# Kernel optimization log

Hardware: AMD Instinct MI355X
Metric: run time of the kernel (lower is better)

The kernel has to match this reference:

```python
import jax, jax.numpy as jnp
from jax import lax
import numpy as np

B, HW, C = 32, 4096, 256
G = 32            # factor / groups
CG = C // G       # per-group channels = 8
EPS = 1e-5


def setup_inputs() -> dict:
    key = jax.random.key(0)
    ks = jax.random.split(key, 7)
    s = 1.0 / np.sqrt(CG)
    s3 = 1.0 / np.sqrt(CG * 9)
    return {
        "x": jax.random.normal(ks[0], (B, HW, C), dtype=jnp.float32),
        "w1": jax.random.uniform(ks[1], (CG, CG), jnp.float32, -s, s),        # conv1x1 weight (O,I)
        "b1": jax.random.uniform(ks[2], (CG,), jnp.float32, -s, s),
        "w3": jax.random.uniform(ks[3], (CG, CG, 3, 3), jnp.float32, -s3, s3),  # conv3x3 weight (O,I,kH,kW)
        "b3": jax.random.uniform(ks[4], (CG,), jnp.float32, -s3, s3),
        "gn_w": jnp.ones((CG,), jnp.float32),
        "gn_b": jnp.zeros((CG,), jnp.float32),
    }


def reference(x, w1, b1, w3, b3, gn_w, gn_b):
    b, hw, c = x.shape
    h = int(np.sqrt(hw)); w = h
    cg = c // G
    n = b * G
    # (b, hw, c) -> (b, c, h, w) -> (b*G, cg, h, w)
    gx = x.transpose(0, 2, 1).reshape(b, c, h, w).reshape(n, cg, h, w)

    # directional pooling
    x_h = gx.mean(axis=3, keepdims=True)                       # (n,cg,h,1)
    x_w = gx.mean(axis=2, keepdims=True).transpose(0, 1, 3, 2)  # (n,cg,w,1)
    cat = jnp.concatenate([x_h, x_w], axis=2)                  # (n,cg,h+w,1)
    # 1x1 conv == channel matmul
    hwm = jnp.einsum('oi,nipq->nopq', w1, cat) + b1[None, :, None, None]
    xh, xw = hwm[:, :, :h], hwm[:, :, h:]

    gated = gx * jax.nn.sigmoid(xh) * jax.nn.sigmoid(xw.transpose(0, 1, 3, 2))

    # GroupNorm(cg groups over cg channels) == per-channel norm over spatial dims
    mu = gated.mean(axis=(2, 3), keepdims=True)
    var = gated.var(axis=(2, 3), keepdims=True)
    x1 = (gated - mu) * lax.rsqrt(var + EPS) * gn_w[None, :, None, None] + gn_b[None, :, None, None]

    x2 = lax.conv_general_dilated(gx, w3, (1, 1), ((1, 1), (1, 1)),
                                  dimension_numbers=('NCHW', 'OIHW', 'NCHW')) + b3[None, :, None, None]

    x11 = jax.nn.softmax(x1.mean(axis=(2, 3)), axis=-1)[:, None, :]  # (n,1,cg)
    x21 = jax.nn.softmax(x2.mean(axis=(2, 3)), axis=-1)[:, None, :]  # (n,1,cg)
    x12 = x2.reshape(n, cg, h * w)
    x22 = x1.reshape(n, cg, h * w)

    weights = (x11 @ x12 + x21 @ x22).reshape(n, 1, h, w)
    out = (gx * jax.nn.sigmoid(weights)).reshape(b, c, h, w)
    return out.reshape(b, c, hw).transpose(0, 2, 1)
```

## Files before the change

### kernel.cpp

```cpp
#include <hip/hip_runtime.h>
#include <math.h>


#define NBLK 1024
#define NTHR 512
#define CSTR 2052

typedef unsigned int uint;

__device__ __forceinline__ uint pk2(float a, float b) {
    uint ua = __builtin_bit_cast(uint, a);
    uint ub = __builtin_bit_cast(uint, b);
    ua = (ua + 0x7FFFu + ((ua >> 16) & 1u)) >> 16;
    ub = (ub + 0x7FFFu + ((ub >> 16) & 1u)) >> 16;
    return ua | (ub << 16);
}
__device__ __forceinline__ float blo(uint u) { return __builtin_bit_cast(float, u << 16); }
__device__ __forceinline__ float bhi(uint u) { return __builtin_bit_cast(float, u & 0xFFFF0000u); }
__device__ __forceinline__ float sigm(float v) { return 1.0f / (1.0f + __expf(-v)); }

__global__ __launch_bounds__(512, 4) void fused_ema_kernel(
    const float* __restrict__ x,
    const float* __restrict__ w1,
    const float* __restrict__ b1,
    const float* __restrict__ w3,
    const float* __restrict__ b3,
    const float* __restrict__ gn_w,
    const float* __restrict__ gn_b,
    float* __restrict__ out)
{
    __shared__ __align__(16) uint  gxp[8 * CSTR];
    __shared__ __align__(16) float sg[8 * 128];
    __shared__ __align__(16) float uni[1024];
    __shared__ __align__(16) float t1s[512];
    __shared__ __align__(16) float weff[96];
    __shared__ float Ti[8], m2s[8], Ai[8], Ci[8], x11s[8], x21s[8];
    __shared__ float wconst_s;

    const int t = threadIdx.x;
    const int bi = blockIdx.x;
    const int n = ((bi & 7) * 32 + ((bi >> 3) >> 2)) * 4 + ((bi >> 3) & 3);
    const int b = n >> 5;
    const int g = n & 31;

    {
        const float4* x4 = reinterpret_cast<const float4*>(x) + (size_t)b * 4096 * 64 + g * 2;
#pragma unroll
        for (int k = 0; k < 8; ++k) {
            int idx = k * 512 + t;
            int q = idx >> 1;
            int half = idx & 1;
            float4 v0 = x4[(size_t)q * 128 + half];
            float4 v1 = x4[(size_t)q * 128 + 64 + half];
            int ch = half * 4;
            gxp[(ch + 0) * CSTR + q] = pk2(v0.x, v1.x);
            gxp[(ch + 1) * CSTR + q] = pk2(v0.y, v1.y);
            gxp[(ch + 2) * CSTR + q] = pk2(v0.z, v1.z);
            gxp[(ch + 3) * CSTR + q] = pk2(v0.w, v1.w);
        }
    }
    __syncthreads();

    float* Rs = uni;
    float* Cs = uni + 512;

    {
        const int i = t >> 6, l = t & 63, ys = l >> 3, xb = l & 7;
        float col[8] = {0, 0, 0, 0, 0, 0, 0, 0};
        float rowv[8];
#pragma unroll
        for (int r = 0; r < 8; ++r) {
            const uint4 d = *reinterpret_cast<const uint4*>(
                &gxp[i * CSTR + (ys * 8 + r) * 32 + xb * 4]);
            float f0 = blo(d.x), f1 = bhi(d.x), f2 = blo(d.y), f3 = bhi(d.y);
            float f4 = blo(d.z), f5 = bhi(d.z), f6 = blo(d.w), f7 = bhi(d.w);
            rowv[r] = ((f0 + f1) + (f2 + f3)) + ((f4 + f5) + (f6 + f7));
            col[0] += f0; col[1] += f1; col[2] += f2; col[3] += f3;
            col[4] += f4; col[5] += f5; col[6] += f6; col[7] += f7;
        }
#pragma unroll
        for (int r = 0; r < 8; ++r) {
            float v = rowv[r];
            v += __shfl_xor(v, 1); v += __shfl_xor(v, 2); v += __shfl_xor(v, 4);
            if (xb == 0) Rs[i * 64 + ys * 8 + r] = v;
        }
        float tot = 0.f;
#pragma unroll
        for (int j = 0; j < 8; ++j) {
            float c = col[j];
            c += __shfl_xor(c, 8); c += __shfl_xor(c, 16); c += __shfl_xor(c, 32);
            if (ys == 0) Cs[i * 64 + xb * 8 + j] = c;
            tot += c;
        }
        tot += __shfl_xor(tot, 1); tot += __shfl_xor(tot, 2); tot += __shfl_xor(tot, 4);
        if (l == 0) Ti[i] = tot;
    }
    __syncthreads();

    {
        const int o = t >> 6, p = t & 63;
        float vy = b1[o], vx = b1[o];
#pragma unroll
        for (int i = 0; i < 8; ++i) {
            float wv = w1[o * 8 + i] * (1.0f / 64.0f);
            vy += wv * Rs[i * 64 + p];
            vx += wv * Cs[i * 64 + p];
        }
        sg[o * 128 + p] = sigm(vy);
        sg[o * 128 + 64 + p] = sigm(vx);
    }
    __syncthreads();

    {
        const int i = t >> 6, l = t & 63, ys = l >> 3, xb = l & 7;
        const float4 sa = *reinterpret_cast<const float4*>(&sg[i * 128 + 64 + xb * 8]);
        const float4 sb = *reinterpret_cast<const float4*>(&sg[i * 128 + 64 + xb * 8 + 4]);
        float s = 0.f, s2 = 0.f;
#pragma unroll
        for (int r = 0; r < 8; ++r) {
            const float shv = sg[i * 128 + ys * 8 + r];
            const uint4 d = *reinterpret_cast<const uint4*>(
                &gxp[i * CSTR + (ys * 8 + r) * 32 + xb * 4]);
            float g0 = blo(d.x) * shv * sa.x; s += g0; s2 += g0 * g0;
            float g1 = bhi(d.x) * shv * sa.y; s += g1; s2 += g1 * g1;
            float g2 = blo(d.y) * shv * sa.z; s += g2; s2 += g2 * g2;
            float g3 = bhi(d.y) * shv * sa.w; s += g3; s2 += g3 * g3;
            float g4 = blo(d.z) * shv * sb.x; s += g4; s2 += g4 * g4;
            float g5 = bhi(d.z) * shv * sb.y; s += g5; s2 += g5 * g5;
            float g6 = blo(d.w) * shv * sb.z; s += g6; s2 += g6 * g6;
            float g7 = bhi(d.w) * shv * sb.w; s += g7; s2 += g7 * g7;
        }
#pragma unroll
        for (int off = 32; off; off >>= 1) {
            s += __shfl_xor(s, off);
            s2 += __shfl_xor(s2, off);
        }
        if (l == 0) {
            float mu = s * (1.0f / 4096.0f);
            float var = s2 * (1.0f / 4096.0f) - mu * mu;
            float a = rsqrtf(var + 1e-5f) * gn_w[i];
            Ai[i] = a;
            Ci[i] = gn_b[i] - mu * a;
        }
    }
    if (t < 64) {
        const int o = t >> 3, i = t & 7;
        const float T = Ti[i];
        float part = 0.f;
#pragma unroll
        for (int ky = 0; ky < 3; ++ky) {
            int dy = ky - 1;
#pragma unroll
            for (int kx = 0; kx < 3; ++kx) {
                int dx = kx - 1;
                float S = T;
                int er = (dy < 0) ? 63 : 0;
                int ec = (dx < 0) ? 63 : 0;
                if (dy != 0) S -= Rs[i * 64 + er];
                if (dx != 0) S -= Cs[i * 64 + ec];
                if (dy != 0 && dx != 0) {
                    uint u = gxp[i * CSTR + er * 32 + (ec >> 1)];
                    S += (ec & 1) ? bhi(u) : blo(u);
                }
                part += w3[((o * 8 + i) * 3 + ky) * 3 + kx] * S;
            }
        }
        part += __shfl_xor(part, 1); part += __shfl_xor(part, 2); part += __shfl_xor(part, 4);
        if (i == 0) m2s[o] = part * (1.0f / 4096.0f) + b3[o];
    }
    if (t < 8) {
        float mx = m2s[0];
#pragma unroll
        for (int o = 1; o < 8; ++o) mx = fmaxf(mx, m2s[o]);
        float sum = 0.f;
#pragma unroll
        for (int o = 0; o < 8; ++o) sum += __expf(m2s[o] - mx);
        x21s[t] = __expf(m2s[t] - mx) / sum;
        float mx1 = gn_b[0];
#pragma unroll
        for (int o = 1; o < 8; ++o) mx1 = fmaxf(mx1, gn_b[o]);
        float sum1 = 0.f;
#pragma unroll
        for (int o = 0; o < 8; ++o) sum1 += __expf(gn_b[o] - mx1);
        x11s[t] = __expf(gn_b[t] - mx1) / sum1;
    }
    __syncthreads();

    if (t < 72) {
        const int i = t / 9, k = t % 9;
        float acc = 0.f;
#pragma unroll
        for (int o = 0; o < 8; ++o) acc += x11s[o] * w3[(o * 8 + i) * 9 + k];
        weff[i * 12 + (k / 3) * 4 + (k % 3)] = acc;
    }
    {
        const int i = t >> 6, y = t & 63;
        t1s[i * 64 + y] = x21s[i] * Ai[i] * sg[i * 128 + y];
    }
    if (t == 0) {
        float wc = 0.f;
#pragma unroll
        for (int o = 0; o < 8; ++o) wc += x11s[o] * b3[o] + x21s[o] * Ci[o];
        wconst_s = wc;
    }
    __syncthreads();

    {
        const int y = t >> 3, xb = t & 7;
        float ws0 = wconst_s, ws1 = wconst_s, ws2 = wconst_s, ws3 = wconst_s;
        float ws4 = wconst_s, ws5 = wconst_s, ws6 = wconst_s, ws7 = wconst_s;
        uint4 gla[8];
#pragma unroll
        for (int i = 0; i < 8; ++i) {
            const float t1v = t1s[i * 64 + y];
            const float4 sa = *reinterpret_cast<const float4*>(&sg[i * 128 + 64 + xb * 8]);
            const float4 sb = *reinterpret_cast<const float4*>(&sg[i * 128 + 64 + xb * 8 + 4]);
#pragma unroll
            for (int dy = -1; dy <= 1; ++dy) {
                const int yy = y + dy;
                if (yy < 0 || yy > 63) continue;
                const uint4 d = *reinterpret_cast<const uint4*>(
                    &gxp[i * CSTR + yy * 32 + xb * 4]);
                float f0 = blo(d.x), f1 = bhi(d.x), f2 = blo(d.y), f3 = bhi(d.y);
                float f4 = blo(d.z), f5 = bhi(d.z), f6 = blo(d.w), f7 = bhi(d.w);
                float vm = __shfl_up(f7, 1);
                float vp = __shfl_down(f0, 1);
                vm = (xb == 0) ? 0.f : vm;
                vp = (xb == 7) ? 0.f : vp;
                const float4 wv = *reinterpret_cast<const float4*>(&weff[i * 12 + (dy + 1) * 4]);
                const float wl = wv.x, wc = wv.y, wr = wv.z;
                ws0 += wl * vm + wc * f0 + wr * f1;
                ws1 += wl * f0 + wc * f1 + wr * f2;
                ws2 += wl * f1 + wc * f2 + wr * f3;
                ws3 += wl * f2 + wc * f3 + wr * f4;
                ws4 += wl * f3 + wc * f4 + wr * f5;
                ws5 += wl * f4 + wc * f5 + wr * f6;
                ws6 += wl * f5 + wc * f6 + wr * f7;
                ws7 += wl * f6 + wc * f7 + wr * vp;
                if (dy == 0) {
                    gla[i] = d;
                    ws0 += t1v * sa.x * f0;  ws1 += t1v * sa.y * f1;
                    ws2 += t1v * sa.z * f2;  ws3 += t1v * sa.w * f3;
                    ws4 += t1v * sb.x * f4;  ws5 += t1v * sb.y * f5;
                    ws6 += t1v * sb.z * f6;  ws7 += t1v * sb.w * f7;
                }
            }
        }
        const float s0 = sigm(ws0), s1 = sigm(ws1), s2 = sigm(ws2), s3 = sigm(ws3);
        const float s4 = sigm(ws4), s5 = sigm(ws5), s6 = sigm(ws6), s7 = sigm(ws7);
        float4* out4 = reinterpret_cast<float4*>(out) + (size_t)b * 4096 * 64 + g * 2;
        const size_t pb = (size_t)(y * 64 + xb * 8) * 64;
        float4 lo, hi;
        lo.x = blo(gla[0].x) * s0; lo.y = blo(gla[1].x) * s0; lo.z = blo(gla[2].x) * s0; lo.w = blo(gla[3].x) * s0;
        hi.x = blo(gla[4].x) * s0; hi.y = blo(gla[5].x) * s0; hi.z = blo(gla[6].x) * s0; hi.w = blo(gla[7].x) * s0;
        out4[pb + 0] = lo; out4[pb + 1] = hi;
        lo.x = bhi(gla[0].x) * s1; lo.y = bhi(gla[1].x) * s1; lo.z = bhi(gla[2].x) * s1; lo.w = bhi(gla[3].x) * s1;
        hi.x = bhi(gla[4].x) * s1; hi.y = bhi(gla[5].x) * s1; hi.z = bhi(gla[6].x) * s1; hi.w = bhi(gla[7].x) * s1;
        out4[pb + 64] = lo; out4[pb + 65] = hi;
        lo.x = blo(gla[0].y) * s2; lo.y = blo(gla[1].y) * s2; lo.z = blo(gla[2].y) * s2; lo.w = blo(gla[3].y) * s2;
        hi.x = blo(gla[4].y) * s2; hi.y = blo(gla[5].y) * s2; hi.z = blo(gla[6].y) * s2; hi.w = blo(gla[7].y) * s2;
        out4[pb + 128] = lo; out4[pb + 129] = hi;
        lo.x = bhi(gla[0].y) * s3; lo.y = bhi(gla[1].y) * s3; lo.z = bhi(gla[2].y) * s3; lo.w = bhi(gla[3].y) * s3;
        hi.x = bhi(gla[4].y) * s3; hi.y = bhi(gla[5].y) * s3; hi.z = bhi(gla[6].y) * s3; hi.w = bhi(gla[7].y) * s3;
        out4[pb + 192] = lo; out4[pb + 193] = hi;
        lo.x = blo(gla[0].z) * s4; lo.y = blo(gla[1].z) * s4; lo.z = blo(gla[2].z) * s4; lo.w = blo(gla[3].z) * s4;
        hi.x = blo(gla[4].z) * s4; hi.y = blo(gla[5].z) * s4; hi.z = blo(gla[6].z) * s4; hi.w = blo(gla[7].z) * s4;
        out4[pb + 256] = lo; out4[pb + 257] = hi;
        lo.x = bhi(gla[0].z) * s5; lo.y = bhi(gla[1].z) * s5; lo.z = bhi(gla[2].z) * s5; lo.w = bhi(gla[3].z) * s5;
        hi.x = bhi(gla[4].z) * s5; hi.y = bhi(gla[5].z) * s5; hi.z = bhi(gla[6].z) * s5; hi.w = bhi(gla[7].z) * s5;
        out4[pb + 320] = lo; out4[pb + 321] = hi;
        lo.x = blo(gla[0].w) * s6; lo.y = blo(gla[1].w) * s6; lo.z = blo(gla[2].w) * s6; lo.w = blo(gla[3].w) * s6;
        hi.x = blo(gla[4].w) * s6; hi.y = blo(gla[5].w) * s6; hi.z = blo(gla[6].w) * s6; hi.w = blo(gla[7].w) * s6;
        out4[pb + 384] = lo; out4[pb + 385] = hi;
        lo.x = bhi(gla[0].w) * s7; lo.y = bhi(gla[1].w) * s7; lo.z = bhi(gla[2].w) * s7; lo.w = bhi(gla[3].w) * s7;
        hi.x = bhi(gla[4].w) * s7; hi.y = bhi(gla[5].w) * s7; hi.z = bhi(gla[6].w) * s7; hi.w = bhi(gla[7].w) * s7;
        out4[pb + 448] = lo; out4[pb + 449] = hi;
    }
}

extern "C" void kernel_launch(void* const* d_in, const int* in_sizes, int n_in,
                              void* d_out, int out_size, void* d_ws, size_t ws_size,
                              hipStream_t stream) {
    const float* x    = (const float*)d_in[0];
    const float* w1   = (const float*)d_in[1];
    const float* b1   = (const float*)d_in[2];
    const float* w3   = (const float*)d_in[3];
    const float* b3   = (const float*)d_in[4];
    const float* gn_w = (const float*)d_in[5];
    const float* gn_b = (const float*)d_in[6];
    float* out = (float*)d_out;

    hipLaunchKernelGGL(fused_ema_kernel, dim3(NBLK), dim3(NTHR), 0, stream,
                       x, w1, b1, w3, b3, gn_w, gn_b, out);
}
```

Measured before the change: 82.94 us.

## Process two groups per block with software-pipelined loads of the second group

Each 1024-thread block now handles two adjacent groups. It loads the second group's input into registers while computing the first group's statistics, then runs the first group's output phase while the second group's statistics are computed. This is meant to hide global-load latency behind compute. The output phase now uses 4 pixels per thread instead of 8, and bf16 rounding in pk2 is simplified to round-half-up. The cost is double the shared memory per block (about 140KB), which limits residency, plus extra registers for the staged loads and a slightly different rounding mode.

```diff
diff --git a/kernel.cpp b/kernel.cpp
--- a/kernel.cpp
+++ b/kernel.cpp
@@ -2,8 +2,8 @@
 #include <math.h>
 
 
-#define NBLK 1024
-#define NTHR 512
+#define NBLK 512
+#define NTHR 1024
 #define CSTR 2052
 
 typedef unsigned int uint;
@@ -11,67 +11,32 @@
 __device__ __forceinline__ uint pk2(float a, float b) {
     uint ua = __builtin_bit_cast(uint, a);
     uint ub = __builtin_bit_cast(uint, b);
-    ua = (ua + 0x7FFFu + ((ua >> 16) & 1u)) >> 16;
-    ub = (ub + 0x7FFFu + ((ub >> 16) & 1u)) >> 16;
-    return ua | (ub << 16);
+    return ((ua + 0x8000u) >> 16) | ((ub + 0x8000u) & 0xFFFF0000u);
 }
 __device__ __forceinline__ float blo(uint u) { return __builtin_bit_cast(float, u << 16); }
 __device__ __forceinline__ float bhi(uint u) { return __builtin_bit_cast(float, u & 0xFFFF0000u); }
 __device__ __forceinline__ float sigm(float v) { return 1.0f / (1.0f + __expf(-v)); }
 
-__global__ __launch_bounds__(512, 4) void fused_ema_kernel(
-    const float* __restrict__ x,
-    const float* __restrict__ w1,
-    const float* __restrict__ b1,
-    const float* __restrict__ w3,
-    const float* __restrict__ b3,
-    const float* __restrict__ gn_w,
-    const float* __restrict__ gn_b,
-    float* __restrict__ out)
+__device__ __forceinline__ void stats_phases(
+    const int t, const uint* __restrict__ tile,
+    float* __restrict__ sg, float* __restrict__ t1s, float* __restrict__ weff,
+    float* __restrict__ wconst, float* __restrict__ uni,
+    float* Ti, float* m2s, float* Ai, float* Ci, float* x11s, float* x21s,
+    const float* __restrict__ w1, const float* __restrict__ b1,
+    const float* __restrict__ w3, const float* __restrict__ b3,
+    const float* __restrict__ gn_w, const float* __restrict__ gn_b)
 {
-    __shared__ __align__(16) uint  gxp[8 * CSTR];
-    __shared__ __align__(16) float sg[8 * 128];
-    __shared__ __align__(16) float uni[1024];
-    __shared__ __align__(16) float t1s[512];
-    __shared__ __align__(16) float weff[96];
-    __shared__ float Ti[8], m2s[8], Ai[8], Ci[8], x11s[8], x21s[8];
-    __shared__ float wconst_s;
-
-    const int t = threadIdx.x;
-    const int bi = blockIdx.x;
-    const int n = ((bi & 7) * 32 + ((bi >> 3) >> 2)) * 4 + ((bi >> 3) & 3);
-    const int b = n >> 5;
-    const int g = n & 31;
-
-    {
-        const float4* x4 = reinterpret_cast<const float4*>(x) + (size_t)b * 4096 * 64 + g * 2;
-#pragma unroll
-        for (int k = 0; k < 8; ++k) {
-            int idx = k * 512 + t;
-            int q = idx >> 1;
-            int half = idx & 1;
-            float4 v0 = x4[(size_t)q * 128 + half];
-            float4 v1 = x4[(size_t)q * 128 + 64 + half];
-            int ch = half * 4;
-            gxp[(ch + 0) * CSTR + q] = pk2(v0.x, v1.x);
-            gxp[(ch + 1) * CSTR + q] = pk2(v0.y, v1.y);
-            gxp[(ch + 2) * CSTR + q] = pk2(v0.z, v1.z);
-            gxp[(ch + 3) * CSTR + q] = pk2(v0.w, v1.w);
-        }
-    }
-    __syncthreads();
-
     float* Rs = uni;
     float* Cs = uni + 512;
 
-    {
+    if (t < 512) {
         const int i = t >> 6, l = t & 63, ys = l >> 3, xb = l & 7;
         float col[8] = {0, 0, 0, 0, 0, 0, 0, 0};
         float rowv[8];
 #pragma unroll
         for (int r = 0; r < 8; ++r) {
             const uint4 d = *reinterpret_cast<const uint4*>(
-                &gxp[i * CSTR + (ys * 8 + r) * 32 + xb * 4]);
+                &tile[i * CSTR + (ys * 8 + r) * 32 + xb * 4]);
             float f0 = blo(d.x), f1 = bhi(d.x), f2 = blo(d.y), f3 = bhi(d.y);
             float f4 = blo(d.z), f5 = bhi(d.z), f6 = blo(d.w), f7 = bhi(d.w);
             rowv[r] = ((f0 + f1) + (f2 + f3)) + ((f4 + f5) + (f6 + f7));
@@ -97,7 +62,7 @@
     }
     __syncthreads();
 
-    {
+    if (t < 512) {
         const int o = t >> 6, p = t & 63;
         float vy = b1[o], vx = b1[o];
 #pragma unroll
@@ -111,7 +76,7 @@
     }
     __syncthreads();
 
-    {
+    if (t < 512) {
         const int i = t >> 6, l = t & 63, ys = l >> 3, xb = l & 7;
         const float4 sa = *reinterpret_cast<const float4*>(&sg[i * 128 + 64 + xb * 8]);
         const float4 sb = *reinterpret_cast<const float4*>(&sg[i * 128 + 64 + xb * 8 + 4]);
@@ -120,7 +85,7 @@
         for (int r = 0; r < 8; ++r) {
             const float shv = sg[i * 128 + ys * 8 + r];
             const uint4 d = *reinterpret_cast<const uint4*>(
-                &gxp[i * CSTR + (ys * 8 + r) * 32 + xb * 4]);
+                &tile[i * CSTR + (ys * 8 + r) * 32 + xb * 4]);
             float g0 = blo(d.x) * shv * sa.x; s += g0; s2 += g0 * g0;
             float g1 = bhi(d.x) * shv * sa.y; s += g1; s2 += g1 * g1;
             float g2 = blo(d.y) * shv * sa.z; s += g2; s2 += g2 * g2;
@@ -159,7 +124,7 @@
                 if (dy != 0) S -= Rs[i * 64 + er];
                 if (dx != 0) S -= Cs[i * 64 + ec];
                 if (dy != 0 && dx != 0) {
-                    uint u = gxp[i * CSTR + er * 32 + (ec >> 1)];
+                    uint u = tile[i * CSTR + er * 32 + (ec >> 1)];
                     S += (ec & 1) ? bhi(u) : blo(u);
                 }
                 part += w3[((o * 8 + i) * 3 + ky) * 3 + kx] * S;
@@ -193,7 +158,7 @@
         for (int o = 0; o < 8; ++o) acc += x11s[o] * w3[(o * 8 + i) * 9 + k];
         weff[i * 12 + (k / 3) * 4 + (k % 3)] = acc;
     }
-    {
+    if (t < 512) {
         const int i = t >> 6, y = t & 63;
         t1s[i * 64 + y] = x21s[i] * Ai[i] * sg[i * 128 + y];
     }
@@ -201,81 +166,147 @@
         float wc = 0.f;
 #pragma unroll
         for (int o = 0; o < 8; ++o) wc += x11s[o] * b3[o] + x21s[o] * Ci[o];
-        wconst_s = wc;
-    }
-    __syncthreads();
+        *wconst = wc;
+    }
+}
+
+__device__ __forceinline__ void apply_phase(
+    const int t, const uint* __restrict__ tile, const float* __restrict__ sg,
+    const float* __restrict__ t1s, const float* __restrict__ weff,
+    const float wconst, float4* __restrict__ out4)
+{
+    const int y = t >> 4, xq = t & 15;
+    float ws0 = wconst, ws1 = wconst, ws2 = wconst, ws3 = wconst;
+    uint2 ctr[8];
+#pragma unroll
+    for (int i = 0; i < 8; ++i) {
+        const float t1v = t1s[i * 64 + y];
+        const float4 sa = *reinterpret_cast<const float4*>(&sg[i * 128 + 64 + xq * 4]);
+#pragma unroll
+        for (int dy = -1; dy <= 1; ++dy) {
+            const int yy = y + dy;
+            if (yy < 0 || yy > 63) continue;
+            const uint2 d = *reinterpret_cast<const uint2*>(
+                &tile[i * CSTR + yy * 32 + xq * 2]);
+            float f0 = blo(d.x), f1 = bhi(d.x), f2 = blo(d.y), f3 = bhi(d.y);
+            float vm = __shfl_up(f3, 1);
+            float vp = __shfl_down(f0, 1);
+            vm = (xq == 0) ? 0.f : vm;
+            vp = (xq == 15) ? 0.f : vp;
+            const float4 wv = *reinterpret_cast<const float4*>(&weff[i * 12 + (dy + 1) * 4]);
+            ws0 += wv.x * vm + wv.y * f0 + wv.z * f1;
+            ws1 += wv.x * f0 + wv.y * f1 + wv.z * f2;
+            ws2 += wv.x * f1 + wv.y * f2 + wv.z * f3;
+            ws3 += wv.x * f2 + wv.y * f3 + wv.z * vp;
+            if (dy == 0) {
+                ctr[i] = d;
+                ws0 += t1v * sa.x * f0;
+                ws1 += t1v * sa.y * f1;
+                ws2 += t1v * sa.z * f2;
+                ws3 += t1v * sa.w * f3;
+            }
+        }
+    }
+    const float s0 = sigm(ws0), s1 = sigm(ws1), s2 = sigm(ws2), s3 = sigm(ws3);
+    const size_t p0 = (size_t)(y * 64 + xq * 4) * 64;
+    float4 u, w;
+    u.x = blo(ctr[0].x) * s0; u.y = blo(ctr[1].x) * s0; u.z = blo(ctr[2].x) * s0; u.w = blo(ctr[3].x) * s0;
+    w.x = blo(ctr[4].x) * s0; w.y = blo(ctr[5].x) * s0; w.z = blo(ctr[6].x) * s0; w.w = blo(ctr[7].x) * s0;
+    out4[p0 + 0] = u; out4[p0 + 1] = w;
+    u.x = bhi(ctr[0].x) * s1; u.y = bhi(ctr[1].x) * s1; u.z = bhi(ctr[2].x) * s1; u.w = bhi(ctr[3].x) * s1;
+    w.x = bhi(ctr[4].x) * s1; w.y = bhi(ctr[5].x) * s1; w.z = bhi(ctr[6].x) * s1; w.w = bhi(ctr[7].x) * s1;
+    out4[p0 + 64] = u; out4[p0 + 65] = w;
+    u.x = blo(ctr[0].y) * s2; u.y = blo(ctr[1].y) * s2; u.z = blo(ctr[2].y) * s2; u.w = blo(ctr[3].y) * s2;
+    w.x = blo(ctr[4].y) * s2; w.y = blo(ctr[5].y) * s2; w.z = blo(ctr[6].y) * s2; w.w = blo(ctr[7].y) * s2;
+    out4[p0 + 128] = u; out4[p0 + 129] = w;
+    u.x = bhi(ctr[0].y) * s3; u.y = bhi(ctr[1].y) * s3; u.z = bhi(ctr[2].y) * s3; u.w = bhi(ctr[3].y) * s3;
+    w.x = bhi(ctr[4].y) * s3; w.y = bhi(ctr[5].y) * s3; w.z = bhi(ctr[6].y) * s3; w.w = bhi(ctr[7].y) * s3;
+    out4[p0 + 192] = u; out4[p0 + 193] = w;
+}
+
+__global__ __launch_bounds__(1024, 4) void fused_ema_pair_kernel(
+    const float* __restrict__ x,
+    const float* __restrict__ w1, const float* __restrict__ b1,
+    const float* __restrict__ w3, const float* __restrict__ b3,
+    const float* __restrict__ gn_w, const float* __restrict__ gn_b,
+    float* __restrict__ out)
+{
+    __shared__ __align__(16) uint  gxp0[8 * CSTR];
+    __shared__ __align__(16) uint  gxp1[8 * CSTR];
+    __shared__ __align__(16) float sg0[1024], sg1[1024];
+    __shared__ __align__(16) float uni[1024];
+    __shared__ __align__(16) float t1s0[512], t1s1[512];
+    __shared__ __align__(16) float weff0[96], weff1[96];
+    __shared__ float Ti[8], m2s[8], Ai[8], Ci[8], x11s[8], x21s[8];
+    __shared__ float wc0, wc1;
+
+    const int t = threadIdx.x;
+    const int bi = blockIdx.x;
+    const int p = (bi & 7) * 64 + (bi >> 3);
+    const int n0 = 2 * p;
+    const int n1 = 2 * p + 1;
+    const int b = n0 >> 5;
+    const int g0 = n0 & 31, g1 = n1 & 31;
+
+    const float4* x40 = reinterpret_cast<const float4*>(x) + (size_t)b * 4096 * 64 + g0 * 2;
+    const float4* x41 = reinterpret_cast<const float4*>(x) + (size_t)b * 4096 * 64 + g1 * 2;
+    float4* out40 = reinterpret_cast<float4*>(out) + (size_t)b * 4096 * 64 + g0 * 2;
+    float4* out41 = reinterpret_cast<float4*>(out) + (size_t)b * 4096 * 64 + g1 * 2;
 
     {
-        const int y = t >> 3, xb = t & 7;
-        float ws0 = wconst_s, ws1 = wconst_s, ws2 = wconst_s, ws3 = wconst_s;
-        float ws4 = wconst_s, ws5 = wconst_s, ws6 = wconst_s, ws7 = wconst_s;
-        uint4 gla[8];
-#pragma unroll
-        for (int i = 0; i < 8; ++i) {
-            const float t1v = t1s[i * 64 + y];
-            const float4 sa = *reinterpret_cast<const float4*>(&sg[i * 128 + 64 + xb * 8]);
-            const float4 sb = *reinterpret_cast<const float4*>(&sg[i * 128 + 64 + xb * 8 + 4]);
-#pragma unroll
-            for (int dy = -1; dy <= 1; ++dy) {
-                const int yy = y + dy;
-                if (yy < 0 || yy > 63) continue;
-                const uint4 d = *reinterpret_cast<const uint4*>(
-                    &gxp[i * CSTR + yy * 32 + xb * 4]);
-                float f0 = blo(d.x), f1 = bhi(d.x), f2 = blo(d.y), f3 = bhi(d.y);
-                float f4 = blo(d.z), f5 = bhi(d.z), f6 = blo(d.w), f7 = bhi(d.w);
-                float vm = __shfl_up(f7, 1);
-                float vp = __shfl_down(f0, 1);
-                vm = (xb == 0) ? 0.f : vm;
-                vp = (xb == 7) ? 0.f : vp;
-                const float4 wv = *reinterpret_cast<const float4*>(&weff[i * 12 + (dy + 1) * 4]);
-                const float wl = wv.x, wc = wv.y, wr = wv.z;
-                ws0 += wl * vm + wc * f0 + wr * f1;
-                ws1 += wl * f0 + wc * f1 + wr * f2;
-                ws2 += wl * f1 + wc * f2 + wr * f3;
-                ws3 += wl * f2 + wc * f3 + wr * f4;
-                ws4 += wl * f3 + wc * f4 + wr * f5;
-                ws5 += wl * f4 + wc * f5 + wr * f6;
-                ws6 += wl * f5 + wc * f6 + wr * f7;
-                ws7 += wl * f6 + wc * f7 + wr * vp;
-                if (dy == 0) {
-                    gla[i] = d;
-                    ws0 += t1v * sa.x * f0;  ws1 += t1v * sa.y * f1;
-                    ws2 += t1v * sa.z * f2;  ws3 += t1v * sa.w * f3;
-                    ws4 += t1v * sb.x * f4;  ws5 += t1v * sb.y * f5;
-                    ws6 += t1v * sb.z * f6;  ws7 += t1v * sb.w * f7;
-                }
-            }
-        }
-        const float s0 = sigm(ws0), s1 = sigm(ws1), s2 = sigm(ws2), s3 = sigm(ws3);
-        const float s4 = sigm(ws4), s5 = sigm(ws5), s6 = sigm(ws6), s7 = sigm(ws7);
-        float4* out4 = reinterpret_cast<float4*>(out) + (size_t)b * 4096 * 64 + g * 2;
-        const size_t pb = (size_t)(y * 64 + xb * 8) * 64;
-        float4 lo, hi;
-        lo.x = blo(gla[0].x) * s0; lo.y = blo(gla[1].x) * s0; lo.z = blo(gla[2].x) * s0; lo.w = blo(gla[3].x) * s0;
-        hi.x = blo(gla[4].x) * s0; hi.y = blo(gla[5].x) * s0; hi.z = blo(gla[6].x) * s0; hi.w = blo(gla[7].x) * s0;
-        out4[pb + 0] = lo; out4[pb + 1] = hi;
-        lo.x = bhi(gla[0].x) * s1; lo.y = bhi(gla[1].x) * s1; lo.z = bhi(gla[2].x) * s1; lo.w = bhi(gla[3].x) * s1;
-        hi.x = bhi(gla[4].x) * s1; hi.y = bhi(gla[5].x) * s1; hi.z = bhi(gla[6].x) * s1; hi.w = bhi(gla[7].x) * s1;
-        out4[pb + 64] = lo; out4[pb + 65] = hi;
-        lo.x = blo(gla[0].y) * s2; lo.y = blo(gla[1].y) * s2; lo.z = blo(gla[2].y) * s2; lo.w = blo(gla[3].y) * s2;
-        hi.x = blo(gla[4].y) * s2; hi.y = blo(gla[5].y) * s2; hi.z = blo(gla[6].y) * s2; hi.w = blo(gla[7].y) * s2;
-        out4[pb + 128] = lo; out4[pb + 129] = hi;
-        lo.x = bhi(gla[0].y) * s3; lo.y = bhi(gla[1].y) * s3; lo.z = bhi(gla[2].y) * s3; lo.w = bhi(gla[3].y) * s3;
-        hi.x = bhi(gla[4].y) * s3; hi.y = bhi(gla[5].y) * s3; hi.z = bhi(gla[6].y) * s3; hi.w = bhi(gla[7].y) * s3;
-        out4[pb + 192] = lo; out4[pb + 193] = hi;
-        lo.x = blo(gla[0].z) * s4; lo.y = blo(gla[1].z) * s4; lo.z = blo(gla[2].z) * s4; lo.w = blo(gla[3].z) * s4;
-        hi.x = blo(gla[4].z) * s4; hi.y = blo(gla[5].z) * s4; hi.z = blo(gla[6].z) * s4; hi.w = blo(gla[7].z) * s4;
-        out4[pb + 256] = lo; out4[pb + 257] = hi;
-        lo.x = bhi(gla[0].z) * s5; lo.y = bhi(gla[1].z) * s5; lo.z = bhi(gla[2].z) * s5; lo.w = bhi(gla[3].z) * s5;
-        hi.x = bhi(gla[4].z) * s5; hi.y = bhi(gla[5].z) * s5; hi.z = bhi(gla[6].z) * s5; hi.w = bhi(gla[7].z) * s5;
-        out4[pb + 320] = lo; out4[pb + 321] = hi;
-        lo.x = blo(gla[0].w) * s6; lo.y = blo(gla[1].w) * s6; lo.z = blo(gla[2].w) * s6; lo.w = blo(gla[3].w) * s6;
-        hi.x = blo(gla[4].w) * s6; hi.y = blo(gla[5].w) * s6; hi.z = blo(gla[6].w) * s6; hi.w = blo(gla[7].w) * s6;
-        out4[pb + 384] = lo; out4[pb + 385] = hi;
-        lo.x = bhi(gla[0].w) * s7; lo.y = bhi(gla[1].w) * s7; lo.z = bhi(gla[2].w) * s7; lo.w = bhi(gla[3].w) * s7;
-        hi.x = bhi(gla[4].w) * s7; hi.y = bhi(gla[5].w) * s7; hi.z = bhi(gla[6].w) * s7; hi.w = bhi(gla[7].w) * s7;
-        out4[pb + 448] = lo; out4[pb + 449] = hi;
-    }
+#pragma unroll
+        for (int k = 0; k < 4; ++k) {
+            int idx = k * 1024 + t;
+            int q = idx >> 1;
+            int half = idx & 1;
+            float4 va = x40[(size_t)q * 128 + half];
+            float4 vb = x40[(size_t)q * 128 + 64 + half];
+            int ch = half * 4;
+            gxp0[(ch + 0) * CSTR + q] = pk2(va.x, vb.x);
+            gxp0[(ch + 1) * CSTR + q] = pk2(va.y, vb.y);
+            gxp0[(ch + 2) * CSTR + q] = pk2(va.z, vb.z);
+            gxp0[(ch + 3) * CSTR + q] = pk2(va.w, vb.w);
+        }
+    }
+    __syncthreads();
+
+    float4 sva[4], svb[4];
+#pragma unroll
+    for (int k = 0; k < 4; ++k) {
+        int idx = k * 1024 + t;
+        int q = idx >> 1;
+        int half = idx & 1;
+        sva[k] = x41[(size_t)q * 128 + half];
+        svb[k] = x41[(size_t)q * 128 + 64 + half];
+    }
+    __builtin_amdgcn_sched_barrier(0);
+
+    stats_phases(t, gxp0, sg0, t1s0, weff0, &wc0, uni,
+                 Ti, m2s, Ai, Ci, x11s, x21s, w1, b1, w3, b3, gn_w, gn_b);
+    __syncthreads();
+
+    {
+#pragma unroll
+        for (int k = 0; k < 4; ++k) {
+            int idx = k * 1024 + t;
+            int q = idx >> 1;
+            int half = idx & 1;
+            int ch = half * 4;
+            gxp1[(ch + 0) * CSTR + q] = pk2(sva[k].x, svb[k].x);
+            gxp1[(ch + 1) * CSTR + q] = pk2(sva[k].y, svb[k].y);
+            gxp1[(ch + 2) * CSTR + q] = pk2(sva[k].z, svb[k].z);
+            gxp1[(ch + 3) * CSTR + q] = pk2(sva[k].w, svb[k].w);
+        }
+    }
+    __syncthreads();
+
+    apply_phase(t, gxp0, sg0, t1s0, weff0, wc0, out40);
+
+    stats_phases(t, gxp1, sg1, t1s1, weff1, &wc1, uni,
+                 Ti, m2s, Ai, Ci, x11s, x21s, w1, b1, w3, b3, gn_w, gn_b);
+    __syncthreads();
+
+    apply_phase(t, gxp1, sg1, t1s1, weff1, wc1, out41);
 }
 
 extern "C" void kernel_launch(void* const* d_in, const int* in_sizes, int n_in,
@@ -290,6 +321,6 @@
     const float* gn_b = (const float*)d_in[6];
     float* out = (float*)d_out;
 
-    hipLaunchKernelGGL(fused_ema_kernel, dim3(NBLK), dim3(NTHR), 0, stream,
+    hipLaunchKernelGGL(fused_ema_pair_kernel, dim3(NBLK), dim3(NTHR), 0, stream,
                        x, w1, b1, w3, b3, gn_w, gn_b, out);
 }
```

Result: slower. 113.6 us (+36.9%).

## Process two groups per block, prefetching the second tile during the first apply phase

Applied to the files above, without the earlier changes.

Halves the grid so each block handles two (batch, group) tiles. While the first tile's apply-and-store phase runs, the block holds the second tile's global loads in registers, hiding load latency behind compute. The bf16 rounding is simplified to round-half-up. The apply phase now reloads the center row from shared memory instead of keeping it in registers, to offset the extra prefetch registers. The risks are higher register pressure with 16 float4 values in flight, and half as many blocks to spread across the GPU.

```diff
diff --git a/kernel.cpp b/kernel.cpp
--- a/kernel.cpp
+++ b/kernel.cpp
@@ -2,7 +2,7 @@
 #include <math.h>
 
 
-#define NBLK 1024
+#define NBLK 512
 #define NTHR 512
 #define CSTR 2052
 
@@ -11,56 +11,40 @@
 __device__ __forceinline__ uint pk2(float a, float b) {
     uint ua = __builtin_bit_cast(uint, a);
     uint ub = __builtin_bit_cast(uint, b);
-    ua = (ua + 0x7FFFu + ((ua >> 16) & 1u)) >> 16;
-    ub = (ub + 0x7FFFu + ((ub >> 16) & 1u)) >> 16;
-    return ua | (ub << 16);
+    return ((ua + 0x8000u) >> 16) | ((ub + 0x8000u) & 0xFFFF0000u);
 }
 __device__ __forceinline__ float blo(uint u) { return __builtin_bit_cast(float, u << 16); }
 __device__ __forceinline__ float bhi(uint u) { return __builtin_bit_cast(float, u & 0xFFFF0000u); }
 __device__ __forceinline__ float sigm(float v) { return 1.0f / (1.0f + __expf(-v)); }
 
-__global__ __launch_bounds__(512, 4) void fused_ema_kernel(
-    const float* __restrict__ x,
-    const float* __restrict__ w1,
-    const float* __restrict__ b1,
-    const float* __restrict__ w3,
-    const float* __restrict__ b3,
-    const float* __restrict__ gn_w,
-    const float* __restrict__ gn_b,
-    float* __restrict__ out)
+__device__ __forceinline__ void load_pack(const int t,
+                                          const float4* __restrict__ x4,
+                                          uint* __restrict__ tile)
 {
-    __shared__ __align__(16) uint  gxp[8 * CSTR];
-    __shared__ __align__(16) float sg[8 * 128];
-    __shared__ __align__(16) float uni[1024];
-    __shared__ __align__(16) float t1s[512];
-    __shared__ __align__(16) float weff[96];
-    __shared__ float Ti[8], m2s[8], Ai[8], Ci[8], x11s[8], x21s[8];
-    __shared__ float wconst_s;
-
-    const int t = threadIdx.x;
-    const int bi = blockIdx.x;
-    const int n = ((bi & 7) * 32 + ((bi >> 3) >> 2)) * 4 + ((bi >> 3) & 3);
-    const int b = n >> 5;
-    const int g = n & 31;
-
-    {
-        const float4* x4 = reinterpret_cast<const float4*>(x) + (size_t)b * 4096 * 64 + g * 2;
-#pragma unroll
-        for (int k = 0; k < 8; ++k) {
-            int idx = k * 512 + t;
-            int q = idx >> 1;
-            int half = idx & 1;
-            float4 v0 = x4[(size_t)q * 128 + half];
-            float4 v1 = x4[(size_t)q * 128 + 64 + half];
-            int ch = half * 4;
-            gxp[(ch + 0) * CSTR + q] = pk2(v0.x, v1.x);
-            gxp[(ch + 1) * CSTR + q] = pk2(v0.y, v1.y);
-            gxp[(ch + 2) * CSTR + q] = pk2(v0.z, v1.z);
-            gxp[(ch + 3) * CSTR + q] = pk2(v0.w, v1.w);
-        }
-    }
-    __syncthreads();
-
+#pragma unroll
+    for (int k = 0; k < 8; ++k) {
+        int idx = k * 512 + t;
+        int q = idx >> 1;
+        int half = idx & 1;
+        float4 va = x4[(size_t)q * 128 + half];
+        float4 vb = x4[(size_t)q * 128 + 64 + half];
+        int ch = half * 4;
+        tile[(ch + 0) * CSTR + q] = pk2(va.x, vb.x);
+        tile[(ch + 1) * CSTR + q] = pk2(va.y, vb.y);
+        tile[(ch + 2) * CSTR + q] = pk2(va.z, vb.z);
+        tile[(ch + 3) * CSTR + q] = pk2(va.w, vb.w);
+    }
+}
+
+__device__ __forceinline__ void stats_phases(
+    const int t, const uint* __restrict__ tile,
+    float* __restrict__ sg, float* __restrict__ t1s, float* __restrict__ weff,
+    float* __restrict__ wconst, float* __restrict__ uni,
+    float* Ti, float* m2s, float* Ai, float* Ci, float* x11s, float* x21s,
+    const float* __restrict__ w1, const float* __restrict__ b1,
+    const float* __restrict__ w3, const float* __restrict__ b3,
+    const float* __restrict__ gn_w, const float* __restrict__ gn_b)
+{
     float* Rs = uni;
     float* Cs = uni + 512;
 
@@ -71,7 +55,7 @@
 #pragma unroll
         for (int r = 0; r < 8; ++r) {
             const uint4 d = *reinterpret_cast<const uint4*>(
-                &gxp[i * CSTR + (ys * 8 + r) * 32 + xb * 4]);
+                &tile[i * CSTR + (ys * 8 + r) * 32 + xb * 4]);
             float f0 = blo(d.x), f1 = bhi(d.x), f2 = blo(d.y), f3 = bhi(d.y);
             float f4 = blo(d.z), f5 = bhi(d.z), f6 = blo(d.w), f7 = bhi(d.w);
             rowv[r] = ((f0 + f1) + (f2 + f3)) + ((f4 + f5) + (f6 + f7));
@@ -120,7 +104,7 @@
         for (int r = 0; r < 8; ++r) {
             const float shv = sg[i * 128 + ys * 8 + r];
             const uint4 d = *reinterpret_cast<const uint4*>(
-                &gxp[i * CSTR + (ys * 8 + r) * 32 + xb * 4]);
+                &tile[i * CSTR + (ys * 8 + r) * 32 + xb * 4]);
             float g0 = blo(d.x) * shv * sa.x; s += g0; s2 += g0 * g0;
             float g1 = bhi(d.x) * shv * sa.y; s += g1; s2 += g1 * g1;
             float g2 = blo(d.y) * shv * sa.z; s += g2; s2 += g2 * g2;
@@ -159,7 +143,7 @@
                 if (dy != 0) S -= Rs[i * 64 + er];
                 if (dx != 0) S -= Cs[i * 64 + ec];
                 if (dy != 0 && dx != 0) {
-                    uint u = gxp[i * CSTR + er * 32 + (ec >> 1)];
+                    uint u = tile[i * CSTR + er * 32 + (ec >> 1)];
                     S += (ec & 1) ? bhi(u) : blo(u);
                 }
                 part += w3[((o * 8 + i) * 3 + ky) * 3 + kx] * S;
@@ -201,81 +185,167 @@
         float wc = 0.f;
 #pragma unroll
         for (int o = 0; o < 8; ++o) wc += x11s[o] * b3[o] + x21s[o] * Ci[o];
-        wconst_s = wc;
-    }
-    __syncthreads();
-
-    {
-        const int y = t >> 3, xb = t & 7;
-        float ws0 = wconst_s, ws1 = wconst_s, ws2 = wconst_s, ws3 = wconst_s;
-        float ws4 = wconst_s, ws5 = wconst_s, ws6 = wconst_s, ws7 = wconst_s;
-        uint4 gla[8];
-#pragma unroll
-        for (int i = 0; i < 8; ++i) {
-            const float t1v = t1s[i * 64 + y];
-            const float4 sa = *reinterpret_cast<const float4*>(&sg[i * 128 + 64 + xb * 8]);
-            const float4 sb = *reinterpret_cast<const float4*>(&sg[i * 128 + 64 + xb * 8 + 4]);
-#pragma unroll
-            for (int dy = -1; dy <= 1; ++dy) {
-                const int yy = y + dy;
-                if (yy < 0 || yy > 63) continue;
-                const uint4 d = *reinterpret_cast<const uint4*>(
-                    &gxp[i * CSTR + yy * 32 + xb * 4]);
-                float f0 = blo(d.x), f1 = bhi(d.x), f2 = blo(d.y), f3 = bhi(d.y);
-                float f4 = blo(d.z), f5 = bhi(d.z), f6 = blo(d.w), f7 = bhi(d.w);
-                float vm = __shfl_up(f7, 1);
-                float vp = __shfl_down(f0, 1);
-                vm = (xb == 0) ? 0.f : vm;
-                vp = (xb == 7) ? 0.f : vp;
-                const float4 wv = *reinterpret_cast<const float4*>(&weff[i * 12 + (dy + 1) * 4]);
-                const float wl = wv.x, wc = wv.y, wr = wv.z;
-                ws0 += wl * vm + wc * f0 + wr * f1;
-                ws1 += wl * f0 + wc * f1 + wr * f2;
-                ws2 += wl * f1 + wc * f2 + wr * f3;
-                ws3 += wl * f2 + wc * f3 + wr * f4;
-                ws4 += wl * f3 + wc * f4 + wr * f5;
-                ws5 += wl * f4 + wc * f5 + wr * f6;
-                ws6 += wl * f5 + wc * f6 + wr * f7;
-                ws7 += wl * f6 + wc * f7 + wr * vp;
-                if (dy == 0) {
-                    gla[i] = d;
-                    ws0 += t1v * sa.x * f0;  ws1 += t1v * sa.y * f1;
-                    ws2 += t1v * sa.z * f2;  ws3 += t1v * sa.w * f3;
-                    ws4 += t1v * sb.x * f4;  ws5 += t1v * sb.y * f5;
-                    ws6 += t1v * sb.z * f6;  ws7 += t1v * sb.w * f7;
-                }
+        *wconst = wc;
+    }
+}
+
+__device__ __forceinline__ void apply_store(
+    const int t, const uint* __restrict__ tile, const float* __restrict__ sg,
+    const float* __restrict__ t1s, const float* __restrict__ weff,
+    const float wconst, float4* __restrict__ out4)
+{
+    const int y = t >> 3, xb = t & 7;
+    float ws0 = wconst, ws1 = wconst, ws2 = wconst, ws3 = wconst;
+    float ws4 = wconst, ws5 = wconst, ws6 = wconst, ws7 = wconst;
+#pragma unroll
+    for (int i = 0; i < 8; ++i) {
+        const float t1v = t1s[i * 64 + y];
+        const float4 sa = *reinterpret_cast<const float4*>(&sg[i * 128 + 64 + xb * 8]);
+        const float4 sb = *reinterpret_cast<const float4*>(&sg[i * 128 + 64 + xb * 8 + 4]);
+#pragma unroll
+        for (int dy = -1; dy <= 1; ++dy) {
+            const int yy = y + dy;
+            if (yy < 0 || yy > 63) continue;
+            const uint4 d = *reinterpret_cast<const uint4*>(
+                &tile[i * CSTR + yy * 32 + xb * 4]);
+            float f0 = blo(d.x), f1 = bhi(d.x), f2 = blo(d.y), f3 = bhi(d.y);
+            float f4 = blo(d.z), f5 = bhi(d.z), f6 = blo(d.w), f7 = bhi(d.w);
+            float vm = __shfl_up(f7, 1);
+            float vp = __shfl_down(f0, 1);
+            vm = (xb == 0) ? 0.f : vm;
+            vp = (xb == 7) ? 0.f : vp;
+            const float4 wv = *reinterpret_cast<const float4*>(&weff[i * 12 + (dy + 1) * 4]);
+            const float wl = wv.x, wc = wv.y, wr = wv.z;
+            ws0 += wl * vm + wc * f0 + wr * f1;
+            ws1 += wl * f0 + wc * f1 + wr * f2;
+            ws2 += wl * f1 + wc * f2 + wr * f3;
+            ws3 += wl * f2 + wc * f3 + wr * f4;
+            ws4 += wl * f3 + wc * f4 + wr * f5;
+            ws5 += wl * f4 + wc * f5 + wr * f6;
+            ws6 += wl * f5 + wc * f6 + wr * f7;
+            ws7 += wl * f6 + wc * f7 + wr * vp;
+            if (dy == 0) {
+                ws0 += t1v * sa.x * f0;  ws1 += t1v * sa.y * f1;
+                ws2 += t1v * sa.z * f2;  ws3 += t1v * sa.w * f3;
+                ws4 += t1v * sb.x * f4;  ws5 += t1v * sb.y * f5;
+                ws6 += t1v * sb.z * f6;  ws7 += t1v * sb.w * f7;
             }
         }
-        const float s0 = sigm(ws0), s1 = sigm(ws1), s2 = sigm(ws2), s3 = sigm(ws3);
-        const float s4 = sigm(ws4), s5 = sigm(ws5), s6 = sigm(ws6), s7 = sigm(ws7);
-        float4* out4 = reinterpret_cast<float4*>(out) + (size_t)b * 4096 * 64 + g * 2;
-        const size_t pb = (size_t)(y * 64 + xb * 8) * 64;
-        float4 lo, hi;
-        lo.x = blo(gla[0].x) * s0; lo.y = blo(gla[1].x) * s0; lo.z = blo(gla[2].x) * s0; lo.w = blo(gla[3].x) * s0;
-        hi.x = blo(gla[4].x) * s0; hi.y = blo(gla[5].x) * s0; hi.z = blo(gla[6].x) * s0; hi.w = blo(gla[7].x) * s0;
-        out4[pb + 0] = lo; out4[pb + 1] = hi;
-        lo.x = bhi(gla[0].x) * s1; lo.y = bhi(gla[1].x) * s1; lo.z = bhi(gla[2].x) * s1; lo.w = bhi(gla[3].x) * s1;
-        hi.x = bhi(gla[4].x) * s1; hi.y = bhi(gla[5].x) * s1; hi.z = bhi(gla[6].x) * s1; hi.w = bhi(gla[7].x) * s1;
-        out4[pb + 64] = lo; out4[pb + 65] = hi;
-        lo.x = blo(gla[0].y) * s2; lo.y = blo(gla[1].y) * s2; lo.z = blo(gla[2].y) * s2; lo.w = blo(gla[3].y) * s2;
-        hi.x = blo(gla[4].y) * s2; hi.y = blo(gla[5].y) * s2; hi.z = blo(gla[6].y) * s2; hi.w = blo(gla[7].y) * s2;
-        out4[pb + 128] = lo; out4[pb + 129] = hi;
-        lo.x = bhi(gla[0].y) * s3; lo.y = bhi(gla[1].y) * s3; lo.z = bhi(gla[2].y) * s3; lo.w = bhi(gla[3].y) * s3;
-        hi.x = bhi(gla[4].y) * s3; hi.y = bhi(gla[5].y) * s3; hi.z = bhi(gla[6].y) * s3; hi.w = bhi(gla[7].y) * s3;
-        out4[pb + 192] = lo; out4[pb + 193] = hi;
-        lo.x = blo(gla[0].z) * s4; lo.y = blo(gla[1].z) * s4; lo.z = blo(gla[2].z) * s4; lo.w = blo(gla[3].z) * s4;
-        hi.x = blo(gla[4].z) * s4; hi.y = blo(gla[5].z) * s4; hi.z = blo(gla[6].z) * s4; hi.w = blo(gla[7].z) * s4;
-        out4[pb + 256] = lo; out4[pb + 257] = hi;
-        lo.x = bhi(gla[0].z) * s5; lo.y = bhi(gla[1].z) * s5; lo.z = bhi(gla[2].z) * s5; lo.w = bhi(gla[3].z) * s5;
-        hi.x = bhi(gla[4].z) * s5; hi.y = bhi(gla[5].z) * s5; hi.z = bhi(gla[6].z) * s5; hi.w = bhi(gla[7].z) * s5;
-        out4[pb + 320] = lo; out4[pb + 321] = hi;
-        lo.x = blo(gla[0].w) * s6; lo.y = blo(gla[1].w) * s6; lo.z = blo(gla[2].w) * s6; lo.w = blo(gla[3].w) * s6;
-        hi.x = blo(gla[4].w) * s6; hi.y = blo(gla[5].w) * s6; hi.z = blo(gla[6].w) * s6; hi.w = blo(gla[7].w) * s6;
-        out4[pb + 384] = lo; out4[pb + 385] = hi;
-        lo.x = bhi(gla[0].w) * s7; lo.y = bhi(gla[1].w) * s7; lo.z = bhi(gla[2].w) * s7; lo.w = bhi(gla[3].w) * s7;
-        hi.x = bhi(gla[4].w) * s7; hi.y = bhi(gla[5].w) * s7; hi.z = bhi(gla[6].w) * s7; hi.w = bhi(gla[7].w) * s7;
-        out4[pb + 448] = lo; out4[pb + 449] = hi;
-    }
+    }
+    const float s0 = sigm(ws0), s1 = sigm(ws1), s2 = sigm(ws2), s3 = sigm(ws3);
+    const float s4 = sigm(ws4), s5 = sigm(ws5), s6 = sigm(ws6), s7 = sigm(ws7);
+    const size_t pb = (size_t)(y * 64 + xb * 8) * 64;
+    {
+        uint4 c0 = *reinterpret_cast<const uint4*>(&tile[0 * CSTR + y * 32 + xb * 4]);
+        uint4 c1 = *reinterpret_cast<const uint4*>(&tile[1 * CSTR + y * 32 + xb * 4]);
+        uint4 c2 = *reinterpret_cast<const uint4*>(&tile[2 * CSTR + y * 32 + xb * 4]);
+        uint4 c3 = *reinterpret_cast<const uint4*>(&tile[3 * CSTR + y * 32 + xb * 4]);
+        float4 v;
+        v.x = blo(c0.x) * s0; v.y = blo(c1.x) * s0; v.z = blo(c2.x) * s0; v.w = blo(c3.x) * s0;
+        out4[pb + 0] = v;
+        v.x = bhi(c0.x) * s1; v.y = bhi(c1.x) * s1; v.z = bhi(c2.x) * s1; v.w = bhi(c3.x) * s1;
+        out4[pb + 64] = v;
+        v.x = blo(c0.y) * s2; v.y = blo(c1.y) * s2; v.z = blo(c2.y) * s2; v.w = blo(c3.y) * s2;
+        out4[pb + 128] = v;
+        v.x = bhi(c0.y) * s3; v.y = bhi(c1.y) * s3; v.z = bhi(c2.y) * s3; v.w = bhi(c3.y) * s3;
+        out4[pb + 192] = v;
+        v.x = blo(c0.z) * s4; v.y = blo(c1.z) * s4; v.z = blo(c2.z) * s4; v.w = blo(c3.z) * s4;
+        out4[pb + 256] = v;
+        v.x = bhi(c0.z) * s5; v.y = bhi(c1.z) * s5; v.z = bhi(c2.z) * s5; v.w = bhi(c3.z) * s5;
+        out4[pb + 320] = v;
+        v.x = blo(c0.w) * s6; v.y = blo(c1.w) * s6; v.z = blo(c2.w) * s6; v.w = blo(c3.w) * s6;
+        out4[pb + 384] = v;
+        v.x = bhi(c0.w) * s7; v.y = bhi(c1.w) * s7; v.z = bhi(c2.w) * s7; v.w = bhi(c3.w) * s7;
+        out4[pb + 448] = v;
+    }
+    {
+        uint4 c4 = *reinterpret_cast<const uint4*>(&tile[4 * CSTR + y * 32 + xb * 4]);
+        uint4 c5 = *reinterpret_cast<const uint4*>(&tile[5 * CSTR + y * 32 + xb * 4]);
+        uint4 c6 = *reinterpret_cast<const uint4*>(&tile[6 * CSTR + y * 32 + xb * 4]);
+        uint4 c7 = *reinterpret_cast<const uint4*>(&tile[7 * CSTR + y * 32 + xb * 4]);
+        float4 v;
+        v.x = blo(c4.x) * s0; v.y = blo(c5.x) * s0; v.z = blo(c6.x) * s0; v.w = blo(c7.x) * s0;
+        out4[pb + 1] = v;
+        v.x = bhi(c4.x) * s1; v.y = bhi(c5.x) * s1; v.z = bhi(c6.x) * s1; v.w = bhi(c7.x) * s1;
+        out4[pb + 65] = v;
+        v.x = blo(c4.y) * s2; v.y = blo(c5.y) * s2; v.z = blo(c6.y) * s2; v.w = blo(c7.y) * s2;
+        out4[pb + 129] = v;
+        v.x = bhi(c4.y) * s3; v.y = bhi(c5.y) * s3; v.z = bhi(c6.y) * s3; v.w = bhi(c7.y) * s3;
+        out4[pb + 193] = v;
+        v.x = blo(c4.z) * s4; v.y = blo(c5.z) * s4; v.z = blo(c6.z) * s4; v.w = blo(c7.z) * s4;
+        out4[pb + 257] = v;
+        v.x = bhi(c4.z) * s5; v.y = bhi(c5.z) * s5; v.z = bhi(c6.z) * s5; v.w = bhi(c7.z) * s5;
+        out4[pb + 321] = v;
+        v.x = blo(c4.w) * s6; v.y = blo(c5.w) * s6; v.z = blo(c6.w) * s6; v.w = blo(c7.w) * s6;
+        out4[pb + 385] = v;
+        v.x = bhi(c4.w) * s7; v.y = bhi(c5.w) * s7; v.z = bhi(c6.w) * s7; v.w = bhi(c7.w) * s7;
+        out4[pb + 449] = v;
+    }
+}
+
+__global__ __launch_bounds__(512, 4) void fused_ema_pipe_kernel(
+    const float* __restrict__ x,
+    const float* __restrict__ w1, const float* __restrict__ b1,
+    const float* __restrict__ w3, const float* __restrict__ b3,
+    const float* __restrict__ gn_w, const float* __restrict__ gn_b,
+    float* __restrict__ out)
+{
+    __shared__ __align__(16) uint  tile[8 * CSTR];
+    __shared__ __align__(16) float sg[1024];
+    __shared__ __align__(16) float uni[1024];
+    __shared__ __align__(16) float t1s[512];
+    __shared__ __align__(16) float weff[96];
+    __shared__ float Ti[8], m2s[8], Ai[8], Ci[8], x11s[8], x21s[8];
+    __shared__ float wcs;
+
+    const int t = threadIdx.x;
+    const int bi = blockIdx.x;
+    const int n0 = ((bi & 7) * 16 + ((bi >> 3) >> 2)) * 4 + ((bi >> 3) & 3);
+    const int b0 = n0 >> 5, g0 = n0 & 31;
+    const int b1v = b0 + 16;
+
+    const float4* x40 = reinterpret_cast<const float4*>(x) + (size_t)b0 * 4096 * 64 + g0 * 2;
+    const float4* x41 = reinterpret_cast<const float4*>(x) + (size_t)b1v * 4096 * 64 + g0 * 2;
+    float4* out40 = reinterpret_cast<float4*>(out) + (size_t)b0 * 4096 * 64 + g0 * 2;
+    float4* out41 = reinterpret_cast<float4*>(out) + (size_t)b1v * 4096 * 64 + g0 * 2;
+
+    load_pack(t, x40, tile);
+    __syncthreads();
+    stats_phases(t, tile, sg, t1s, weff, &wcs, uni,
+                 Ti, m2s, Ai, Ci, x11s, x21s, w1, b1, w3, b3, gn_w, gn_b);
+    __syncthreads();
+
+    float4 va[8], vb[8];
+#pragma unroll
+    for (int k = 0; k < 8; ++k) {
+        int idx = k * 512 + t;
+        int q = idx >> 1;
+        int half = idx & 1;
+        va[k] = x41[(size_t)q * 128 + half];
+        vb[k] = x41[(size_t)q * 128 + 64 + half];
+    }
+    __builtin_amdgcn_sched_barrier(0);
+
+    apply_store(t, tile, sg, t1s, weff, wcs, out40);
+    __syncthreads();
+
+#pragma unroll
+    for (int k = 0; k < 8; ++k) {
+        int idx = k * 512 + t;
+        int q = idx >> 1;
+        int half = idx & 1;
+        int ch = half * 4;
+        tile[(ch + 0) * CSTR + q] = pk2(va[k].x, vb[k].x);
+        tile[(ch + 1) * CSTR + q] = pk2(va[k].y, vb[k].y);
+        tile[(ch + 2) * CSTR + q] = pk2(va[k].z, vb[k].z);
+        tile[(ch + 3) * CSTR + q] = pk2(va[k].w, vb[k].w);
+    }
+    __syncthreads();
+
+    stats_phases(t, tile, sg, t1s, weff, &wcs, uni,
+                 Ti, m2s, Ai, Ci, x11s, x21s, w1, b1, w3, b3, gn_w, gn_b);
+    __syncthreads();
+    apply_store(t, tile, sg, t1s, weff, wcs, out41);
 }
 
 extern "C" void kernel_launch(void* const* d_in, const int* in_sizes, int n_in,
@@ -290,6 +360,6 @@
     const float* gn_b = (const float*)d_in[6];
     float* out = (float*)d_out;
 
-    hipLaunchKernelGGL(fused_ema_kernel, dim3(NBLK), dim3(NTHR), 0, stream,
+    hipLaunchKernelGGL(fused_ema_pipe_kernel, dim3(NBLK), dim3(NTHR), 0, stream,
                        x, w1, b1, w3, b3, gn_w, gn_b, out);
 }
```

New measurement: 136.5 us. 64.5% more time.
